# Optimization experiments

Hardware: AMD Instinct MI355X
Metric: run time of the kernel (lower is better)

Reference implementation:

```python
import jax, jax.numpy as jnp
import numpy as np

B, IN, H, OUT, L = 65536, 784, 64, 10, 8  # batch, input, hidden, output, num_layers


def setup_inputs() -> dict:
    key = jax.random.key(0)
    ks = jax.random.split(key, 10)
    u = lambda k, shape, fan_in: jax.random.uniform(k, shape, jnp.float32,
                                                    -1.0 / np.sqrt(fan_in), 1.0 / np.sqrt(fan_in))
    return {
        "x": jax.random.normal(ks[0], (B, IN), jnp.float32),
        "W0": u(ks[1], (H, IN), IN),
        "b0": u(ks[2], (H,), IN),
        "Wh": u(ks[3], (L - 1, H, H), H),   # layers[1..L-1]
        "bh": u(ks[4], (L - 1, H), H),
        "Wp": u(ks[5], (L * (L - 1), H, H), H),  # weights_past
        "Wf": u(ks[6], (L * (L - 1), H, H), H),  # weights_future
        "Wout": u(ks[7], (OUT, H), H),
        "bout": u(ks[8], (OUT,), H),
    }


def _forward(x, W0, b0, Wh, bh, Wp, Wf, Wout, bout):
    nl = Wh.shape[0] + 1  # num_layers
    x = x.reshape(x.shape[0], -1)
    h = jax.nn.silu(x @ W0.T + b0)
    outputs = [h]
    for i in range(1, nl):
        # past_weighted_sum: sum_j<i (Wp[j*(L-1)+(i-1)] @ outputs[j].T).T == outputs[j] @ Wp[...].T
        past = sum(outputs[j] @ Wp[j * (nl - 1) + (i - 1)].T for j in range(i))
        h = jax.nn.silu(past @ Wh[i - 1].T + bh[i - 1])
        outputs.append(h)
        future_terms = []
        for j in range(i + 1, nl):
            fw = sum(outputs[k] @ Wf[k * (nl - 1) + (j - 1)].T for k in range(i + 1))
            future_terms.append(fw)
        if future_terms:
            h = h + sum(future_terms)
            outputs[-1] = h
    logits = outputs[-1] @ Wout.T + bout
    return jax.nn.log_softmax(logits, axis=1)


def reference(x, W0, b0, Wh, bh, Wp, Wf, Wout, bout):
    return _forward(x, W0, b0, Wh, bh, Wp, Wf, Wout, bout)
```

## Files before the change

kernel.cpp:

```cpp
#include <hip/hip_runtime.h>
#include <hip/hip_fp16.h>


typedef _Float16 half8 __attribute__((ext_vector_type(8)));
typedef float    f32x4 __attribute__((ext_vector_type(4)));

constexpr int MAT_OFF  = 0;
constexpr int W0F_OFF  = 55 * 8192;
constexpr int WOUT_OFF = W0F_OFF + 25 * 4096;
constexpr int S0_OFF   = WOUT_OFF + 4096;

__host__ __device__ constexpr int cIdx(int i, int j) { return (i - 1) * i / 2 + j; }
__host__ __device__ constexpr int fOff(int i) {
    return (i == 1) ? 0 : (i == 2) ? 2 : (i == 3) ? 5 : (i == 4) ? 9 : (i == 5) ? 14 : 20;
}
__host__ __device__ constexpr int fIdx(int i, int k) { return 28 + fOff(i) + k; }

__device__ __forceinline__ float fast_silu(float v) {
    return v * __builtin_amdgcn_rcpf(1.f + __expf(-v));
}

__device__ __forceinline__ void loadTerm(half8 (&buf)[8], const half8* __restrict__ wm,
                                         int slot, int lane) {
#pragma unroll
    for (int q = 0; q < 8; ++q) buf[q] = wm[slot * 512 + q * 64 + lane];
}

__device__ __forceinline__ void term16(const half8 (&bfs)[8], const half8 (&a0)[2],
                                       const half8 (&a1)[2], f32x4 (&c0)[4], f32x4 (&c1)[4]) {
#pragma unroll
    for (int c = 0; c < 4; ++c)
#pragma unroll
        for (int h = 0; h < 2; ++h) {
            const half8 bf = bfs[c * 2 + h];
            c0[c] = __builtin_amdgcn_mfma_f32_16x16x32_f16(a0[h], bf, c0[c], 0, 0, 0);
            c1[c] = __builtin_amdgcn_mfma_f32_16x16x32_f16(a1[h], bf, c1[c], 0, 0, 0);
        }
}

__device__ __forceinline__ void dToA(_Float16* sw, int lane, const f32x4* v, half8* out) {
    const int m = lane & 15, g = lane >> 4;
#pragma unroll
    for (int c = 0; c < 4; ++c) {
        const int kh = c >> 1;
        const int lp = (2 * (c & 1) + (m >> 3)) << 4;
#pragma unroll
        for (int j = 0; j < 4; ++j) {
            const int X = lp + 4 * g + j;
            sw[kh * 512 + ((X ^ (X >> 3)) << 3) + (m & 7)] = (_Float16)v[c][j];
        }
    }
    const int ls = (lane ^ (lane >> 3)) << 3;
    out[0] = *(const half8*)(sw + ls);
    out[1] = *(const half8*)(sw + 512 + ls);
}

__global__ void prep_mats(const float* __restrict__ Wh, const float* __restrict__ Wp,
                          const float* __restrict__ Wf, char* __restrict__ wsb) {
    __shared__ float M[64][64];
    const int b = blockIdx.x, tid = threadIdx.x;
    const int m = tid >> 2, q = tid & 3;
    float acc[16];
#pragma unroll
    for (int u = 0; u < 16; ++u) acc[u] = 0.f;

    if (b < 28) {
        int i = 1;
        while (i < 7 && i * (i + 1) / 2 <= b) ++i;
        const int j = b - (i - 1) * i / 2;
        const float* wh = Wh + (size_t)(i - 1) * 4096;
        const float* wp = Wp + (size_t)(j * 7 + (i - 1)) * 4096;
#pragma unroll 4
        for (int t = 0; t < 64; ++t) {
            const float a = wh[m * 64 + t];
            const f32x4* r = (const f32x4*)(wp + t * 64 + q * 16);
            const f32x4 r0 = r[0], r1 = r[1], r2 = r[2], r3 = r[3];
#pragma unroll
            for (int u = 0; u < 4; ++u) {
                acc[u]      += a * r0[u];
                acc[4 + u]  += a * r1[u];
                acc[8 + u]  += a * r2[u];
                acc[12 + u] += a * r3[u];
            }
        }
    } else {
        const int rr = b - 28;
        int i = 1;
        while (i < 6 && fOff(i + 1) <= rr) ++i;
        const int k = rr - fOff(i);
        for (int jj = i + 1; jj <= 7; ++jj) {
            const f32x4* wf = (const f32x4*)(Wf + (size_t)(k * 7 + (jj - 1)) * 4096 + m * 64 + q * 16);
            const f32x4 r0 = wf[0], r1 = wf[1], r2 = wf[2], r3 = wf[3];
#pragma unroll
            for (int u = 0; u < 4; ++u) {
                acc[u]      += r0[u];
                acc[4 + u]  += r1[u];
                acc[8 + u]  += r2[u];
                acc[12 + u] += r3[u];
            }
        }
        if (k == i) {
#pragma unroll
            for (int u = 0; u < 16; ++u) acc[u] += (m == q * 16 + u) ? 1.0f : 0.0f;
        }
    }
#pragma unroll
    for (int u = 0; u < 16; ++u) M[m][q * 16 + u] = acc[u];
    __syncthreads();

    const int lane = tid & 63;
#pragma unroll
    for (int rep = 0; rep < 2; ++rep) {
        const int qq = (tid >> 6) + rep * 4;
        const int c = qq >> 1, h = qq & 1;
        const int rowM = c * 16 + (lane & 15);
        const int kb = h * 32 + (lane >> 4) * 8;
        half8 o;
#pragma unroll
        for (int e = 0; e < 8; ++e) o[e] = (_Float16)M[rowM][kb + e];
        *(half8*)(wsb + MAT_OFF + (size_t)b * 8192 + qq * 1024 + lane * 16) = o;
    }
}

__global__ void prep_w0(const float* __restrict__ W0, const float* __restrict__ Wout,
                        char* __restrict__ wsb) {
    const int b = blockIdx.x, tid = threadIdx.x;
    const int lane = tid & 63;
    if (b < 25) {
        const int c = tid >> 6;
        const int rowW = c * 16 + (lane & 15);
        const int kb = b * 32 + (lane >> 4) * 8;
        half8 o;
#pragma unroll
        for (int e = 0; e < 8; ++e) {
            const int k = kb + e;
            o[e] = (k < 784) ? (_Float16)W0[(size_t)rowW * 784 + k] : (_Float16)0.f;
        }
        *(half8*)(wsb + W0F_OFF + (size_t)(b * 4 + c) * 1024 + lane * 16) = o;
    } else {
        if (tid < 128) {
            const int h = tid >> 6;
            const int mcol = lane & 15;
            const int kb = h * 32 + (lane >> 4) * 8;
            half8 o;
#pragma unroll
            for (int e = 0; e < 8; ++e)
                o[e] = (mcol < 10) ? (_Float16)Wout[mcol * 64 + kb + e] : (_Float16)0.f;
            *(half8*)(wsb + WOUT_OFF + (size_t)(h * 64 + lane) * 16) = o;
        }
    }
}

__global__ __launch_bounds__(256, 4) void layer0(const float* __restrict__ x,
                                                 const float* __restrict__ b0,
                                                 char* __restrict__ wsb) {
    __shared__ __align__(16) _Float16 scr0[4][1024];
    const int tid = threadIdx.x, lane = tid & 63, wv = tid >> 6;
    const int rt = blockIdx.x * 4 + wv;
    const int m = lane & 15, g = lane >> 4;
    const float* xrow = x + (size_t)(rt * 16 + m) * 784;
    const int ko = g * 8;
    const half8* w0f = (const half8*)(wsb + W0F_OFF);

    f32x4 acc[4];
#pragma unroll
    for (int c = 0; c < 4; ++c) acc[c] = (f32x4){0.f, 0.f, 0.f, 0.f};

#pragma unroll
    for (int t = 0; t < 24; ++t) {
        const f32x4 u0 = *(const f32x4*)(xrow + t * 32 + ko);
        const f32x4 u1 = *(const f32x4*)(xrow + t * 32 + ko + 4);
        half8 a;
#pragma unroll
        for (int e = 0; e < 4; ++e) { a[e] = (_Float16)u0[e]; a[4 + e] = (_Float16)u1[e]; }
#pragma unroll
        for (int c = 0; c < 4; ++c)
            acc[c] = __builtin_amdgcn_mfma_f32_16x16x32_f16(a, w0f[(t * 4 + c) * 64 + lane],
                                                            acc[c], 0, 0, 0);
    }
    {
        half8 a;
#pragma unroll
        for (int e = 0; e < 8; ++e) a[e] = (_Float16)0.f;
        if (ko < 16) {
            const f32x4 u0 = *(const f32x4*)(xrow + 768 + ko);
            const f32x4 u1 = *(const f32x4*)(xrow + 768 + ko + 4);
#pragma unroll
            for (int e = 0; e < 4; ++e) { a[e] = (_Float16)u0[e]; a[4 + e] = (_Float16)u1[e]; }
        }
#pragma unroll
        for (int c = 0; c < 4; ++c)
            acc[c] = __builtin_amdgcn_mfma_f32_16x16x32_f16(a, w0f[(24 * 4 + c) * 64 + lane],
                                                            acc[c], 0, 0, 0);
    }
#pragma unroll
    for (int c = 0; c < 4; ++c) {
        const float bb = b0[c * 16 + m];
#pragma unroll
        for (int j = 0; j < 4; ++j)
            acc[c][j] = fast_silu(acc[c][j] + bb);
    }
    half8 sA[2];
    dToA(&scr0[wv][0], lane, acc, sA);
    char* s0 = wsb + S0_OFF + (size_t)rt * 2048;
    *(half8*)(s0 + lane * 16) = sA[0];
    *(half8*)(s0 + 1024 + lane * 16) = sA[1];
}

__global__ __launch_bounds__(256, 2) void layersB(const float* __restrict__ bh,
                                                  const float* __restrict__ bout,
                                                  const char* __restrict__ wsb,
                                                  float* __restrict__ dOut) {
    __shared__ __align__(16) _Float16 scrh[4][2][1024];
    const int tid = threadIdx.x, lane = tid & 63, wv = tid >> 6;
    const int rt2 = blockIdx.x * 4 + wv;
    const int m = lane & 15, g = lane >> 4;
    _Float16* sw0 = &scrh[wv][0][0];
    _Float16* sw1 = &scrh[wv][1][0];
    const half8* wm = (const half8*)(wsb + MAT_OFF);

    half8 stA[8][2][2];
#pragma unroll
    for (int t = 0; t < 2; ++t) {
        const char* s0 = wsb + S0_OFF + (size_t)(rt2 * 2 + t) * 2048;
        stA[0][t][0] = *(const half8*)(s0 + lane * 16);
        stA[0][t][1] = *(const half8*)(s0 + 1024 + lane * 16);
    }

    half8 pf0[8], pf1[8];
    loadTerm(pf0, wm, cIdx(1, 0), lane);

    f32x4 accL[2];
    accL[0] = (f32x4){0.f, 0.f, 0.f, 0.f};
    accL[1] = (f32x4){0.f, 0.f, 0.f, 0.f};

#pragma unroll
    for (int i = 1; i < 8; ++i) {
        const int nb = i * i - 1;
        f32x4 acc[2][4];
#pragma unroll
        for (int c = 0; c < 4; ++c) {
            const float bb = bh[(i - 1) * 64 + c * 16 + m];
            acc[0][c] = (f32x4){bb, bb, bb, bb};
            acc[1][c] = (f32x4){bb, bb, bb, bb};
        }
#pragma unroll
        for (int tc = 0; tc < i; ++tc) {
            const bool hn = (tc + 1 < i) || (i < 7);
            const int ns = (tc + 1 < i) ? cIdx(i, tc + 1) : (i < 7 ? fIdx(i, 0) : 0);
            if (((nb + tc) & 1) == 0) {
                if (hn) loadTerm(pf1, wm, ns, lane);
                term16(pf0, stA[tc][0], stA[tc][1], acc[0], acc[1]);
            } else {
                if (hn) loadTerm(pf0, wm, ns, lane);
                term16(pf1, stA[tc][0], stA[tc][1], acc[0], acc[1]);
            }
        }
#pragma unroll
        for (int t = 0; t < 2; ++t)
#pragma unroll
            for (int c = 0; c < 4; ++c)
#pragma unroll
                for (int j = 0; j < 4; ++j)
                    acc[t][c][j] = fast_silu(acc[t][c][j]);
        half8 sA[2][2];
        dToA(sw0, lane, acc[0], sA[0]);
        dToA(sw1, lane, acc[1], sA[1]);

        if (i < 7) {
            f32x4 accO[2][4];
#pragma unroll
            for (int t = 0; t < 2; ++t)
#pragma unroll
                for (int c = 0; c < 4; ++c) accO[t][c] = (f32x4){0.f, 0.f, 0.f, 0.f};
#pragma unroll
            for (int k = 0; k < i; ++k) {
                const int ns = (k + 1 < i) ? fIdx(i, k + 1) : fIdx(i, i);
                if (((nb + i + k) & 1) == 0) {
                    loadTerm(pf1, wm, ns, lane);
                    term16(pf0, stA[k][0], stA[k][1], accO[0], accO[1]);
                } else {
                    loadTerm(pf0, wm, ns, lane);
                    term16(pf1, stA[k][0], stA[k][1], accO[0], accO[1]);
                }
            }
            {
                const int ns = cIdx(i + 1, 0);
                if (((nb + 2 * i) & 1) == 0) {
                    loadTerm(pf1, wm, ns, lane);
                    term16(pf0, sA[0], sA[1], accO[0], accO[1]);
                } else {
                    loadTerm(pf0, wm, ns, lane);
                    term16(pf1, sA[0], sA[1], accO[0], accO[1]);
                }
            }
            dToA(sw0, lane, accO[0], &stA[i][0][0]);
            dToA(sw1, lane, accO[1], &stA[i][1][0]);
        } else {
            const half8* wo = (const half8*)(wsb + WOUT_OFF);
            const half8 wo0 = wo[lane], wo1 = wo[64 + lane];
#pragma unroll
            for (int t = 0; t < 2; ++t) {
                accL[t] = __builtin_amdgcn_mfma_f32_16x16x32_f16(sA[t][0], wo0, accL[t], 0, 0, 0);
                accL[t] = __builtin_amdgcn_mfma_f32_16x16x32_f16(sA[t][1], wo1, accL[t], 0, 0, 0);
            }
        }
    }

    const float bb = (m < 10) ? bout[m] : 0.f;
#pragma unroll
    for (int t = 0; t < 2; ++t)
#pragma unroll
        for (int j = 0; j < 4; ++j) {
            const float logit = accL[t][j] + bb;
            float mx = (m < 10) ? logit : -1e30f;
#pragma unroll
            for (int d = 1; d < 16; d <<= 1) mx = fmaxf(mx, __shfl_xor(mx, d, 16));
            const float e = (m < 10) ? __expf(logit - mx) : 0.f;
            float sum = e;
#pragma unroll
            for (int d = 1; d < 16; d <<= 1) sum += __shfl_xor(sum, d, 16);
            const float ls = logit - mx - __logf(sum);
            if (m < 10) dOut[(size_t)(rt2 * 32 + t * 16 + 4 * g + j) * 10 + m] = ls;
        }
}

extern "C" void kernel_launch(void* const* d_in, const int* in_sizes, int n_in,
                              void* d_out, int out_size, void* d_ws, size_t ws_size,
                              hipStream_t stream) {
    (void)in_sizes; (void)n_in; (void)out_size; (void)ws_size;
    const float* x    = (const float*)d_in[0];
    const float* W0   = (const float*)d_in[1];
    const float* b0   = (const float*)d_in[2];
    const float* Wh   = (const float*)d_in[3];
    const float* bh   = (const float*)d_in[4];
    const float* Wp   = (const float*)d_in[5];
    const float* Wf   = (const float*)d_in[6];
    const float* Wout = (const float*)d_in[7];
    const float* bout = (const float*)d_in[8];
    char* wsb = (char*)d_ws;
    float* out = (float*)d_out;

    hipLaunchKernelGGL(prep_mats, dim3(55), dim3(256), 0, stream, Wh, Wp, Wf, wsb);
    hipLaunchKernelGGL(prep_w0,   dim3(26), dim3(256), 0, stream, W0, Wout, wsb);
    hipLaunchKernelGGL(layer0,    dim3(1024), dim3(256), 0, stream, x, b0, wsb);
    hipLaunchKernelGGL(layersB,   dim3(512),  dim3(256), 0, stream, bh, bout, wsb, out);
}
```

Baseline: 389.9 us.

## Fuse layer0 into main MLP kernel and merge prep kernels into one launch

Merges the two weight-prep kernels into a single prep_all launch and splits the Wh·Wp product blocks four ways so more blocks work in parallel. Fuses the first layer (x @ W0, SiLU) into the main layer kernel, so the per-row layer-0 activations never round-trip through global workspace, and drops one launch. It also reorders the future-term accumulation so the current layer's term runs first, and hoists the Wout load. The fused kernel carries more registers for two row tiles during layer 0, which may affect occupancy.

```diff
diff --git a/kernel.cpp b/kernel.cpp
--- a/kernel.cpp
+++ b/kernel.cpp
@@ -8,7 +8,6 @@
 constexpr int MAT_OFF  = 0;
 constexpr int W0F_OFF  = 55 * 8192;
 constexpr int WOUT_OFF = W0F_OFF + 25 * 4096;
-constexpr int S0_OFF   = WOUT_OFF + 4096;
 
 __host__ __device__ constexpr int cIdx(int i, int j) { return (i - 1) * i / 2 + j; }
 __host__ __device__ constexpr int fOff(int i) {
@@ -55,39 +54,48 @@
     out[1] = *(const half8*)(sw + 512 + ls);
 }
 
-__global__ void prep_mats(const float* __restrict__ Wh, const float* __restrict__ Wp,
-                          const float* __restrict__ Wf, char* __restrict__ wsb) {
+__global__ void prep_all(const float* __restrict__ W0, const float* __restrict__ Wout,
+                         const float* __restrict__ Wh, const float* __restrict__ Wp,
+                         const float* __restrict__ Wf, char* __restrict__ wsb) {
     __shared__ float M[64][64];
     const int b = blockIdx.x, tid = threadIdx.x;
-    const int m = tid >> 2, q = tid & 3;
-    float acc[16];
-#pragma unroll
-    for (int u = 0; u < 16; ++u) acc[u] = 0.f;
-
-    if (b < 28) {
+    const int lane = tid & 63, wv = tid >> 6;
+
+    if (b < 112) {
+        const int ci = b >> 2, c = b & 3;
         int i = 1;
-        while (i < 7 && i * (i + 1) / 2 <= b) ++i;
-        const int j = b - (i - 1) * i / 2;
-        const float* wh = Wh + (size_t)(i - 1) * 4096;
+        while (i < 7 && i * (i + 1) / 2 <= ci) ++i;
+        const int j = ci - (i - 1) * i / 2;
+        const int r = tid >> 4, q4 = tid & 15;
+        const float* wh = Wh + (size_t)(i - 1) * 4096 + (c * 16 + r) * 64;
         const float* wp = Wp + (size_t)(j * 7 + (i - 1)) * 4096;
+        float a4[4] = {0.f, 0.f, 0.f, 0.f};
 #pragma unroll 4
         for (int t = 0; t < 64; ++t) {
-            const float a = wh[m * 64 + t];
-            const f32x4* r = (const f32x4*)(wp + t * 64 + q * 16);
-            const f32x4 r0 = r[0], r1 = r[1], r2 = r[2], r3 = r[3];
-#pragma unroll
-            for (int u = 0; u < 4; ++u) {
-                acc[u]      += a * r0[u];
-                acc[4 + u]  += a * r1[u];
-                acc[8 + u]  += a * r2[u];
-                acc[12 + u] += a * r3[u];
-            }
-        }
-    } else {
-        const int rr = b - 28;
+            const float a = wh[t];
+            const f32x4 r0 = *(const f32x4*)(wp + t * 64 + q4 * 4);
+#pragma unroll
+            for (int u = 0; u < 4; ++u) a4[u] += a * r0[u];
+        }
+#pragma unroll
+        for (int u = 0; u < 4; ++u) M[r][q4 * 4 + u] = a4[u];
+        __syncthreads();
+        if (wv < 2) {
+            const int kb = wv * 32 + (lane >> 4) * 8;
+            half8 o;
+#pragma unroll
+            for (int e = 0; e < 8; ++e) o[e] = (_Float16)M[lane & 15][kb + e];
+            *(half8*)(wsb + MAT_OFF + (size_t)ci * 8192 + (2 * c + wv) * 1024 + lane * 16) = o;
+        }
+    } else if (b < 139) {
+        const int rr = b - 112;
         int i = 1;
         while (i < 6 && fOff(i + 1) <= rr) ++i;
         const int k = rr - fOff(i);
+        const int m = tid >> 2, q = tid & 3;
+        float acc[16];
+#pragma unroll
+        for (int u = 0; u < 16; ++u) acc[u] = 0.f;
         for (int jj = i + 1; jj <= 7; ++jj) {
             const f32x4* wf = (const f32x4*)(Wf + (size_t)(k * 7 + (jj - 1)) * 4096 + m * 64 + q * 16);
             const f32x4 r0 = wf[0], r1 = wf[1], r2 = wf[2], r3 = wf[3];
@@ -103,40 +111,32 @@
 #pragma unroll
             for (int u = 0; u < 16; ++u) acc[u] += (m == q * 16 + u) ? 1.0f : 0.0f;
         }
-    }
-#pragma unroll
-    for (int u = 0; u < 16; ++u) M[m][q * 16 + u] = acc[u];
-    __syncthreads();
-
-    const int lane = tid & 63;
-#pragma unroll
-    for (int rep = 0; rep < 2; ++rep) {
-        const int qq = (tid >> 6) + rep * 4;
-        const int c = qq >> 1, h = qq & 1;
-        const int rowM = c * 16 + (lane & 15);
-        const int kb = h * 32 + (lane >> 4) * 8;
-        half8 o;
-#pragma unroll
-        for (int e = 0; e < 8; ++e) o[e] = (_Float16)M[rowM][kb + e];
-        *(half8*)(wsb + MAT_OFF + (size_t)b * 8192 + qq * 1024 + lane * 16) = o;
-    }
-}
-
-__global__ void prep_w0(const float* __restrict__ W0, const float* __restrict__ Wout,
-                        char* __restrict__ wsb) {
-    const int b = blockIdx.x, tid = threadIdx.x;
-    const int lane = tid & 63;
-    if (b < 25) {
-        const int c = tid >> 6;
+#pragma unroll
+        for (int u = 0; u < 16; ++u) M[m][q * 16 + u] = acc[u];
+        __syncthreads();
+        const int slot = 28 + rr;
+#pragma unroll
+        for (int rep = 0; rep < 2; ++rep) {
+            const int qq = wv + rep * 4;
+            const int cc = qq >> 1, h = qq & 1;
+            const int kb = h * 32 + (lane >> 4) * 8;
+            half8 o;
+#pragma unroll
+            for (int e = 0; e < 8; ++e) o[e] = (_Float16)M[cc * 16 + (lane & 15)][kb + e];
+            *(half8*)(wsb + MAT_OFF + (size_t)slot * 8192 + qq * 1024 + lane * 16) = o;
+        }
+    } else if (b < 164) {
+        const int bb = b - 139;
+        const int c = wv;
         const int rowW = c * 16 + (lane & 15);
-        const int kb = b * 32 + (lane >> 4) * 8;
+        const int kb = bb * 32 + (lane >> 4) * 8;
         half8 o;
 #pragma unroll
         for (int e = 0; e < 8; ++e) {
             const int k = kb + e;
             o[e] = (k < 784) ? (_Float16)W0[(size_t)rowW * 784 + k] : (_Float16)0.f;
         }
-        *(half8*)(wsb + W0F_OFF + (size_t)(b * 4 + c) * 1024 + lane * 16) = o;
+        *(half8*)(wsb + W0F_OFF + (size_t)(bb * 4 + c) * 1024 + lane * 16) = o;
     } else {
         if (tid < 128) {
             const int h = tid >> 6;
@@ -151,88 +151,93 @@
     }
 }
 
-__global__ __launch_bounds__(256, 4) void layer0(const float* __restrict__ x,
-                                                 const float* __restrict__ b0,
-                                                 char* __restrict__ wsb) {
-    __shared__ __align__(16) _Float16 scr0[4][1024];
-    const int tid = threadIdx.x, lane = tid & 63, wv = tid >> 6;
-    const int rt = blockIdx.x * 4 + wv;
-    const int m = lane & 15, g = lane >> 4;
-    const float* xrow = x + (size_t)(rt * 16 + m) * 784;
-    const int ko = g * 8;
-    const half8* w0f = (const half8*)(wsb + W0F_OFF);
-
-    f32x4 acc[4];
-#pragma unroll
-    for (int c = 0; c < 4; ++c) acc[c] = (f32x4){0.f, 0.f, 0.f, 0.f};
-
-#pragma unroll
-    for (int t = 0; t < 24; ++t) {
-        const f32x4 u0 = *(const f32x4*)(xrow + t * 32 + ko);
-        const f32x4 u1 = *(const f32x4*)(xrow + t * 32 + ko + 4);
-        half8 a;
-#pragma unroll
-        for (int e = 0; e < 4; ++e) { a[e] = (_Float16)u0[e]; a[4 + e] = (_Float16)u1[e]; }
-#pragma unroll
-        for (int c = 0; c < 4; ++c)
-            acc[c] = __builtin_amdgcn_mfma_f32_16x16x32_f16(a, w0f[(t * 4 + c) * 64 + lane],
-                                                            acc[c], 0, 0, 0);
-    }
-    {
-        half8 a;
-#pragma unroll
-        for (int e = 0; e < 8; ++e) a[e] = (_Float16)0.f;
-        if (ko < 16) {
-            const f32x4 u0 = *(const f32x4*)(xrow + 768 + ko);
-            const f32x4 u1 = *(const f32x4*)(xrow + 768 + ko + 4);
-#pragma unroll
-            for (int e = 0; e < 4; ++e) { a[e] = (_Float16)u0[e]; a[4 + e] = (_Float16)u1[e]; }
-        }
-#pragma unroll
-        for (int c = 0; c < 4; ++c)
-            acc[c] = __builtin_amdgcn_mfma_f32_16x16x32_f16(a, w0f[(24 * 4 + c) * 64 + lane],
-                                                            acc[c], 0, 0, 0);
-    }
-#pragma unroll
-    for (int c = 0; c < 4; ++c) {
-        const float bb = b0[c * 16 + m];
-#pragma unroll
-        for (int j = 0; j < 4; ++j)
-            acc[c][j] = fast_silu(acc[c][j] + bb);
-    }
-    half8 sA[2];
-    dToA(&scr0[wv][0], lane, acc, sA);
-    char* s0 = wsb + S0_OFF + (size_t)rt * 2048;
-    *(half8*)(s0 + lane * 16) = sA[0];
-    *(half8*)(s0 + 1024 + lane * 16) = sA[1];
-}
-
-__global__ __launch_bounds__(256, 2) void layersB(const float* __restrict__ bh,
-                                                  const float* __restrict__ bout,
-                                                  const char* __restrict__ wsb,
-                                                  float* __restrict__ dOut) {
+__global__ __launch_bounds__(256, 2) void mlp_fused(const float* __restrict__ x,
+                                                    const float* __restrict__ b0,
+                                                    const float* __restrict__ bh,
+                                                    const float* __restrict__ bout,
+                                                    const char* __restrict__ wsb,
+                                                    float* __restrict__ dOut) {
     __shared__ __align__(16) _Float16 scrh[4][2][1024];
     const int tid = threadIdx.x, lane = tid & 63, wv = tid >> 6;
     const int rt2 = blockIdx.x * 4 + wv;
+    const int rowBase = rt2 * 32;
     const int m = lane & 15, g = lane >> 4;
     _Float16* sw0 = &scrh[wv][0][0];
     _Float16* sw1 = &scrh[wv][1][0];
     const half8* wm = (const half8*)(wsb + MAT_OFF);
 
     half8 stA[8][2][2];
-#pragma unroll
-    for (int t = 0; t < 2; ++t) {
-        const char* s0 = wsb + S0_OFF + (size_t)(rt2 * 2 + t) * 2048;
-        stA[0][t][0] = *(const half8*)(s0 + lane * 16);
-        stA[0][t][1] = *(const half8*)(s0 + 1024 + lane * 16);
-    }
-
     half8 pf0[8], pf1[8];
     loadTerm(pf0, wm, cIdx(1, 0), lane);
+
+    {
+        const float* xr0 = x + (size_t)(rowBase + m) * 784;
+        const float* xr1 = x + (size_t)(rowBase + 16 + m) * 784;
+        const int ko = g * 8;
+        const half8* w0f = (const half8*)(wsb + W0F_OFF);
+        f32x4 acc[2][4];
+#pragma unroll
+        for (int t = 0; t < 2; ++t)
+#pragma unroll
+            for (int c = 0; c < 4; ++c) acc[t][c] = (f32x4){0.f, 0.f, 0.f, 0.f};
+#pragma unroll
+        for (int t = 0; t < 24; ++t) {
+            const f32x4 u0 = *(const f32x4*)(xr0 + t * 32 + ko);
+            const f32x4 u1 = *(const f32x4*)(xr0 + t * 32 + ko + 4);
+            const f32x4 v0 = *(const f32x4*)(xr1 + t * 32 + ko);
+            const f32x4 v1 = *(const f32x4*)(xr1 + t * 32 + ko + 4);
+            half8 a0, a1;
+#pragma unroll
+            for (int e = 0; e < 4; ++e) {
+                a0[e] = (_Float16)u0[e]; a0[4 + e] = (_Float16)u1[e];
+                a1[e] = (_Float16)v0[e]; a1[4 + e] = (_Float16)v1[e];
+            }
+#pragma unroll
+            for (int c = 0; c < 4; ++c) {
+                const half8 bf = w0f[(t * 4 + c) * 64 + lane];
+                acc[0][c] = __builtin_amdgcn_mfma_f32_16x16x32_f16(a0, bf, acc[0][c], 0, 0, 0);
+                acc[1][c] = __builtin_amdgcn_mfma_f32_16x16x32_f16(a1, bf, acc[1][c], 0, 0, 0);
+            }
+        }
+        {
+            half8 a0, a1;
+#pragma unroll
+            for (int e = 0; e < 8; ++e) { a0[e] = (_Float16)0.f; a1[e] = (_Float16)0.f; }
+            if (ko < 16) {
+                const f32x4 u0 = *(const f32x4*)(xr0 + 768 + ko);
+                const f32x4 u1 = *(const f32x4*)(xr0 + 768 + ko + 4);
+                const f32x4 v0 = *(const f32x4*)(xr1 + 768 + ko);
+                const f32x4 v1 = *(const f32x4*)(xr1 + 768 + ko + 4);
+#pragma unroll
+                for (int e = 0; e < 4; ++e) {
+                    a0[e] = (_Float16)u0[e]; a0[4 + e] = (_Float16)u1[e];
+                    a1[e] = (_Float16)v0[e]; a1[4 + e] = (_Float16)v1[e];
+                }
+            }
+#pragma unroll
+            for (int c = 0; c < 4; ++c) {
+                const half8 bf = w0f[(24 * 4 + c) * 64 + lane];
+                acc[0][c] = __builtin_amdgcn_mfma_f32_16x16x32_f16(a0, bf, acc[0][c], 0, 0, 0);
+                acc[1][c] = __builtin_amdgcn_mfma_f32_16x16x32_f16(a1, bf, acc[1][c], 0, 0, 0);
+            }
+        }
+#pragma unroll
+        for (int t = 0; t < 2; ++t)
+#pragma unroll
+            for (int c = 0; c < 4; ++c) {
+                const float bb = b0[c * 16 + m];
+#pragma unroll
+                for (int jj = 0; jj < 4; ++jj)
+                    acc[t][c][jj] = fast_silu(acc[t][c][jj] + bb);
+            }
+        dToA(sw0, lane, acc[0], stA[0][0]);
+        dToA(sw1, lane, acc[1], stA[0][1]);
+    }
 
     f32x4 accL[2];
     accL[0] = (f32x4){0.f, 0.f, 0.f, 0.f};
     accL[1] = (f32x4){0.f, 0.f, 0.f, 0.f};
+    half8 wo0, wo1;
 
 #pragma unroll
     for (int i = 1; i < 8; ++i) {
@@ -247,7 +252,7 @@
 #pragma unroll
         for (int tc = 0; tc < i; ++tc) {
             const bool hn = (tc + 1 < i) || (i < 7);
-            const int ns = (tc + 1 < i) ? cIdx(i, tc + 1) : (i < 7 ? fIdx(i, 0) : 0);
+            const int ns = (tc + 1 < i) ? cIdx(i, tc + 1) : (i < 7 ? fIdx(i, i) : 0);
             if (((nb + tc) & 1) == 0) {
                 if (hn) loadTerm(pf1, wm, ns, lane);
                 term16(pf0, stA[tc][0], stA[tc][1], acc[0], acc[1]);
@@ -261,8 +266,12 @@
 #pragma unroll
             for (int c = 0; c < 4; ++c)
 #pragma unroll
-                for (int j = 0; j < 4; ++j)
-                    acc[t][c][j] = fast_silu(acc[t][c][j]);
+                for (int jj = 0; jj < 4; ++jj)
+                    acc[t][c][jj] = fast_silu(acc[t][c][jj]);
+        if (i == 7) {
+            const half8* wo = (const half8*)(wsb + WOUT_OFF);
+            wo0 = wo[lane]; wo1 = wo[64 + lane];
+        }
         half8 sA[2][2];
         dToA(sw0, lane, acc[0], sA[0]);
         dToA(sw1, lane, acc[1], sA[1]);
@@ -273,10 +282,20 @@
             for (int t = 0; t < 2; ++t)
 #pragma unroll
                 for (int c = 0; c < 4; ++c) accO[t][c] = (f32x4){0.f, 0.f, 0.f, 0.f};
+            {
+                const int ns = fIdx(i, 0);
+                if (((nb + i) & 1) == 0) {
+                    loadTerm(pf1, wm, ns, lane);
+                    term16(pf0, sA[0], sA[1], accO[0], accO[1]);
+                } else {
+                    loadTerm(pf0, wm, ns, lane);
+                    term16(pf1, sA[0], sA[1], accO[0], accO[1]);
+                }
+            }
 #pragma unroll
             for (int k = 0; k < i; ++k) {
-                const int ns = (k + 1 < i) ? fIdx(i, k + 1) : fIdx(i, i);
-                if (((nb + i + k) & 1) == 0) {
+                const int ns = (k + 1 < i) ? fIdx(i, k + 1) : cIdx(i + 1, 0);
+                if (((nb + i + 1 + k) & 1) == 0) {
                     loadTerm(pf1, wm, ns, lane);
                     term16(pf0, stA[k][0], stA[k][1], accO[0], accO[1]);
                 } else {
@@ -284,21 +303,9 @@
                     term16(pf1, stA[k][0], stA[k][1], accO[0], accO[1]);
                 }
             }
-            {
-                const int ns = cIdx(i + 1, 0);
-                if (((nb + 2 * i) & 1) == 0) {
-                    loadTerm(pf1, wm, ns, lane);
-                    term16(pf0, sA[0], sA[1], accO[0], accO[1]);
-                } else {
-                    loadTerm(pf0, wm, ns, lane);
-                    term16(pf1, sA[0], sA[1], accO[0], accO[1]);
-                }
-            }
             dToA(sw0, lane, accO[0], &stA[i][0][0]);
             dToA(sw1, lane, accO[1], &stA[i][1][0]);
         } else {
-            const half8* wo = (const half8*)(wsb + WOUT_OFF);
-            const half8 wo0 = wo[lane], wo1 = wo[64 + lane];
 #pragma unroll
             for (int t = 0; t < 2; ++t) {
                 accL[t] = __builtin_amdgcn_mfma_f32_16x16x32_f16(sA[t][0], wo0, accL[t], 0, 0, 0);
@@ -311,8 +318,8 @@
 #pragma unroll
     for (int t = 0; t < 2; ++t)
 #pragma unroll
-        for (int j = 0; j < 4; ++j) {
-            const float logit = accL[t][j] + bb;
+        for (int jj = 0; jj < 4; ++jj) {
+            const float logit = accL[t][jj] + bb;
             float mx = (m < 10) ? logit : -1e30f;
 #pragma unroll
             for (int d = 1; d < 16; d <<= 1) mx = fmaxf(mx, __shfl_xor(mx, d, 16));
@@ -321,7 +328,7 @@
 #pragma unroll
             for (int d = 1; d < 16; d <<= 1) sum += __shfl_xor(sum, d, 16);
             const float ls = logit - mx - __logf(sum);
-            if (m < 10) dOut[(size_t)(rt2 * 32 + t * 16 + 4 * g + j) * 10 + m] = ls;
+            if (m < 10) dOut[(size_t)(rowBase + t * 16 + 4 * g + jj) * 10 + m] = ls;
         }
 }
 
@@ -341,8 +348,6 @@
     char* wsb = (char*)d_ws;
     float* out = (float*)d_out;
 
-    hipLaunchKernelGGL(prep_mats, dim3(55), dim3(256), 0, stream, Wh, Wp, Wf, wsb);
-    hipLaunchKernelGGL(prep_w0,   dim3(26), dim3(256), 0, stream, W0, Wout, wsb);
-    hipLaunchKernelGGL(layer0,    dim3(1024), dim3(256), 0, stream, x, b0, wsb);
-    hipLaunchKernelGGL(layersB,   dim3(512),  dim3(256), 0, stream, bh, bout, wsb, out);
-}
+    hipLaunchKernelGGL(prep_all,  dim3(165), dim3(256), 0, stream, W0, Wout, Wh, Wp, Wf, wsb);
+    hipLaunchKernelGGL(mlp_fused, dim3(512), dim3(256), 0, stream, x, b0, bh, bout, wsb, out);
+}
```

Result: faster. 360.1 us (-7.6%).
